# Performance work log

Measured on AMD Instinct MI355X. Metric: run time of the kernel, lower is better.

## Reference

```python
import jax, jax.numpy as jnp
import numpy as np

N, P, DEG, K, H, FIN, EPS = 65536, 64, 16, 3, 64, 16, 1e-5
E = N * DEG
G = N // P


def _bn(x, g, b):
    # BatchNorm1d, training mode: batch stats over the node dim
    mu = jnp.mean(x, axis=0)
    var = jnp.mean((x - mu) ** 2, axis=0)
    return g * (x - mu) * jax.lax.rsqrt(var + EPS) + b


def setup_inputs() -> dict:
    key = jax.random.key(0)
    ks = jax.random.split(key, 16)
    feat = jax.random.normal(ks[0], (N, FIN), jnp.float32)
    # 1024 graphs of 64 nodes, fixed in-degree DEG, edges stay within each graph
    dst = jnp.repeat(jnp.arange(N, dtype=jnp.int32), DEG)
    src = (dst // P) * P + jax.random.randint(ks[1], (E,), 0, P, jnp.int32)
    graph_ids = jnp.arange(N, dtype=jnp.int32) // P
    s = 0.1
    d = dict(feat=feat, src=src, dst=dst, graph_ids=graph_ids)
    d['cheb1_w'] = jax.random.normal(ks[2], (H, K * FIN), jnp.float32) * s
    d['cheb1_b'] = jnp.zeros((H,), jnp.float32)
    d['bn1_g'] = jnp.ones((H,), jnp.float32)
    d['bn1_b'] = jnp.zeros((H,), jnp.float32)
    d['e1_tw'] = jax.random.normal(ks[3], (H, H), jnp.float32) * s
    d['e1_tb'] = jnp.zeros((H,), jnp.float32)
    d['e1_pw'] = jax.random.normal(ks[4], (H, H), jnp.float32) * s
    d['e1_pb'] = jnp.zeros((H,), jnp.float32)
    d['bne1_g'] = jnp.ones((H,), jnp.float32)
    d['bne1_b'] = jnp.zeros((H,), jnp.float32)
    d['cheb2_w'] = jax.random.normal(ks[5], (H, K * H), jnp.float32) * s
    d['cheb2_b'] = jnp.zeros((H,), jnp.float32)
    d['bn2_g'] = jnp.ones((H,), jnp.float32)
    d['bn2_b'] = jnp.zeros((H,), jnp.float32)
    d['e2_tw'] = jax.random.normal(ks[6], (H, H), jnp.float32) * s
    d['e2_tb'] = jnp.zeros((H,), jnp.float32)
    d['e2_pw'] = jax.random.normal(ks[7], (H, H), jnp.float32) * s
    d['e2_pb'] = jnp.zeros((H,), jnp.float32)
    d['bne2_g'] = jnp.ones((H,), jnp.float32)
    d['bne2_b'] = jnp.zeros((H,), jnp.float32)
    d['cheb3_w'] = jax.random.normal(ks[8], (H, K * H), jnp.float32) * s
    d['cheb3_b'] = jnp.zeros((H,), jnp.float32)
    d['bn3_g'] = jnp.ones((H,), jnp.float32)
    d['bn3_b'] = jnp.zeros((H,), jnp.float32)
    return d


def _forward(feat, src, dst, graph_ids,
             cheb1_w, cheb1_b, bn1_g, bn1_b,
             e1_tw, e1_tb, e1_pw, e1_pb, bne1_g, bne1_b,
             cheb2_w, cheb2_b, bn2_g, bn2_b,
             e2_tw, e2_tb, e2_pw, e2_pb, bne2_g, bne2_b,
             cheb3_w, cheb3_b, bn3_g, bn3_b):
    # symmetric norm from in-degrees (DGL ChebConv), clamp(min=1)
    deg = jax.ops.segment_sum(jnp.ones((E,), jnp.float32), dst, num_segments=N)
    dinv = jnp.maximum(deg, 1.0) ** -0.5  # [N]
    dinv = dinv[:, None]

    def lap(f):  # A_hat @ f = D^-1/2 A D^-1/2 f  (messages src -> dst)
        return jax.ops.segment_sum((f * dinv)[src], dst, num_segments=N) * dinv

    def cheb(x, w, b):
        # lambda_max = 2 (DGL default) => re_norm = 1, L_hat = -A_hat
        X0 = x
        X1 = -lap(X0)
        Xs = [X0, X1]
        for _ in range(K - 2):
            Xi = -2.0 * lap(X1) - X0  # T_k = 2 L_hat T_{k-1} - T_{k-2}
            Xs.append(Xi)
            X0, X1 = X1, Xi
        return jnp.concatenate(Xs, axis=1) @ w.T + b

    def econv(x, tw, tb, pw, pb):
        # DGL EdgeConv: max_j [ theta(x_dst - x_src) + phi(x_dst) ]
        m = (x[dst] - x[src]) @ tw.T + tb + (x @ pw.T + pb)[dst]  # [E,H]
        agg = jax.ops.segment_max(m, dst, num_segments=N)
        return jnp.where(jnp.isfinite(agg), agg, 0.0)

    h = jax.nn.relu(_bn(cheb(feat, cheb1_w, cheb1_b), bn1_g, bn1_b))
    h = jax.nn.relu(_bn(econv(h, e1_tw, e1_tb, e1_pw, e1_pb), bne1_g, bne1_b))
    h = jax.nn.relu(_bn(cheb(h, cheb2_w, cheb2_b), bn2_g, bn2_b))
    h = jax.nn.relu(_bn(econv(h, e2_tw, e2_tb, e2_pw, e2_pb), bne2_g, bne2_b))
    h = jax.nn.relu(_bn(cheb(h, cheb3_w, cheb3_b), bn3_g, bn3_b))
    # dgl.mean_nodes: per-graph mean readout
    sums = jax.ops.segment_sum(h, graph_ids, num_segments=G)
    cnt = jax.ops.segment_sum(jnp.ones((N,), jnp.float32), graph_ids, num_segments=G)
    return sums / cnt[:, None]


def reference(feat, src, dst, graph_ids,
              cheb1_w, cheb1_b, bn1_g, bn1_b,
              e1_tw, e1_tb, e1_pw, e1_pb, bne1_g, bne1_b,
              cheb2_w, cheb2_b, bn2_g, bn2_b,
              e2_tw, e2_tb, e2_pw, e2_pb, bne2_g, bne2_b,
              cheb3_w, cheb3_b, bn3_g, bn3_b):
    return _forward(feat, src, dst, graph_ids,
                    cheb1_w, cheb1_b, bn1_g, bn1_b,
                    e1_tw, e1_tb, e1_pw, e1_pb, bne1_g, bne1_b,
                    cheb2_w, cheb2_b, bn2_g, bn2_b,
                    e2_tw, e2_tb, e2_pw, e2_pb, bne2_g, bne2_b,
                    cheb3_w, cheb3_b, bn3_g, bn3_b)
```

## Files before the change

### kernel.cpp

```cpp
#include <hip/hip_runtime.h>

#define NN 65536
#define PP 64
#define HH 64
#define FINN 16
#define NG 1024
#define EPSF 1e-5f
#define C1 0.0625f
#define NREP 32

typedef short bf16x8 __attribute__((ext_vector_type(8)));
typedef short s16x4 __attribute__((ext_vector_type(4)));
typedef float f32x4 __attribute__((ext_vector_type(4)));
typedef unsigned short u16;

#define MFMA(a, b, c) __builtin_amdgcn_mfma_f32_16x16x32_bf16(a, b, c, 0, 0, 0)

__device__ __forceinline__ u16 f2bf(float x) {
  union { float f; unsigned u; } v; v.f = x; return (u16)(v.u >> 16);
}
__device__ __forceinline__ float bf2f(u16 h) {
  union { float f; unsigned u; } v; v.u = ((unsigned)h) << 16; return v.f;
}
__device__ __forceinline__ void split2(float x, u16& h, u16& l) {
  h = f2bf(x); l = f2bf(x - bf2f(h));
}
__device__ __forceinline__ int XIDX(int r, int c) {
  return r * 64 + ((((c >> 3) ^ (r & 7)) << 3) | (c & 7));
}

__device__ __forceinline__ void rep_reduce(const float* __restrict__ stats_in,
                                           int t, float* sstats) {
  if (t < 128) {
    float s = 0.f;
    const float* p = stats_in + t;
#pragma unroll
    for (int r = 0; r < NREP; r++) s += p[r * 128];
    sstats[t] = s;
  }
}

__device__ __forceinline__ void build_adj(const int* __restrict__ src, int g,
                                          int r, u16* Adj) {
  bf16x8 z = {0, 0, 0, 0, 0, 0, 0, 0};
#pragma unroll
  for (int q = 0; q < 8; q++) *(bf16x8*)&Adj[r * 64 + q * 8] = z;
  const int4* s4 = (const int4*)(src + (size_t)g * 1024 + (size_t)r * 16);
  int4 a0 = s4[0], a1 = s4[1], a2 = s4[2], a3 = s4[3];
  int b0 = g * 64;
  int ss[16] = {a0.x - b0, a0.y - b0, a0.z - b0, a0.w - b0,
                a1.x - b0, a1.y - b0, a1.z - b0, a1.w - b0,
                a2.x - b0, a2.y - b0, a2.z - b0, a2.w - b0,
                a3.x - b0, a3.y - b0, a3.z - b0, a3.w - b0};
#pragma unroll
  for (int e = 0; e < 16; e++) {
    int idx = XIDX(r, ss[e]);
    Adj[idx] = f2bf(bf2f(Adj[idx]) + 1.0f);
  }
}

__device__ __forceinline__ void stage_load(const float* __restrict__ y_in,
                                           int g, int t, float4* v) {
  int n = t >> 2, c0 = (t & 3) * 16;
  const float* yr = y_in + ((size_t)(g * 64 + n)) * 64 + c0;
#pragma unroll
  for (int q = 0; q < 4; q++) v[q] = ((const float4*)yr)[q];
}

__device__ __forceinline__ void stage_bn2(
    const float4* v, const float* sstats, const float* __restrict__ gam,
    const float* __restrict__ bet, int t, u16* NMh, u16* NMl, u16* CMh,
    u16* CMl) {
  const float inv = 1.0f / (float)NN;
  int n = t >> 2, c0 = (t & 3) * 16;
  u16 hh[16], ll[16];
#pragma unroll
  for (int q = 0; q < 4; q++) {
#pragma unroll
    for (int k = 0; k < 4; k++) {
      int c = c0 + q * 4 + k;
      float s1 = sstats[c], s2 = sstats[64 + c];
      float mu = s1 * inv;
      float var = fmaf(s2, inv, -mu * mu);
      float sc = gam[c] * rsqrtf(var + EPSF);
      float sh = fmaf(-mu, sc, bet[c]);
      float x = (k == 0) ? v[q].x : (k == 1) ? v[q].y : (k == 2) ? v[q].z
                                                                 : v[q].w;
      float h = fmaxf(fmaf(sc, x, sh), 0.f);
      split2(h, hh[q * 4 + k], ll[q * 4 + k]);
    }
  }
  bf16x8 vh0, vh1, vl0, vl1;
#pragma unroll
  for (int k = 0; k < 8; k++) {
    vh0[k] = (short)hh[k]; vl0[k] = (short)ll[k];
    vh1[k] = (short)hh[8 + k]; vl1[k] = (short)ll[8 + k];
  }
  *(bf16x8*)&NMh[XIDX(n, c0)] = vh0;
  *(bf16x8*)&NMh[XIDX(n, c0 + 8)] = vh1;
  *(bf16x8*)&NMl[XIDX(n, c0)] = vl0;
  *(bf16x8*)&NMl[XIDX(n, c0 + 8)] = vl1;
  if (CMh) {
#pragma unroll
    for (int k = 0; k < 16; k++) {
      CMh[XIDX(c0 + k, n)] = hh[k];
      CMl[XIDX(c0 + k, n)] = ll[k];
    }
  }
}

__device__ __forceinline__ void epilogue(f32x4 a0, f32x4 a1, f32x4 a2, f32x4 a3,
                                         const float* __restrict__ bias, int g,
                                         int w, int ml, int kq,
                                         float* __restrict__ y_out,
                                         float* __restrict__ stats_out) {
  float4 bb = *(const float4*)(bias + w * 16 + kq * 4);
  float s1[4] = {0, 0, 0, 0}, s2[4] = {0, 0, 0, 0};
#pragma unroll
  for (int nt = 0; nt < 4; nt++) {
    f32x4 A = (nt == 0) ? a0 : (nt == 1) ? a1 : (nt == 2) ? a2 : a3;
    float4 yv;
    yv.x = A[0] + bb.x; yv.y = A[1] + bb.y;
    yv.z = A[2] + bb.z; yv.w = A[3] + bb.w;
    int n = nt * 16 + ml;
    *(float4*)(y_out + ((size_t)(g * 64 + n)) * 64 + w * 16 + kq * 4) = yv;
    s1[0] += yv.x; s2[0] += yv.x * yv.x;
    s1[1] += yv.y; s2[1] += yv.y * yv.y;
    s1[2] += yv.z; s2[2] += yv.z * yv.z;
    s1[3] += yv.w; s2[3] += yv.w * yv.w;
  }
#pragma unroll
  for (int i = 0; i < 4; i++) {
#pragma unroll
    for (int off = 1; off < 16; off <<= 1) {
      s1[i] += __shfl_xor(s1[i], off, 64);
      s2[i] += __shfl_xor(s2[i], off, 64);
    }
  }
  if (ml == 0) {
    float* pr = stats_out + (size_t)(g & (NREP - 1)) * 128 + w * 16 + kq * 4;
    atomicAdd(pr + 0, s1[0]);
    atomicAdd(pr + 1, s1[1]);
    atomicAdd(pr + 2, s1[2]);
    atomicAdd(pr + 3, s1[3]);
    atomicAdd(pr + 64, s2[0]);
    atomicAdd(pr + 65, s2[1]);
    atomicAdd(pr + 66, s2[2]);
    atomicAdd(pr + 67, s2[3]);
  }
}

__global__ __launch_bounds__(256, 2) void k_cheb64(
    const float* __restrict__ y_in, const float* __restrict__ stats_in,
    const float* __restrict__ gam, const float* __restrict__ bet,
    const int* __restrict__ src, const u16* __restrict__ wh,
    const u16* __restrict__ wl, const float* __restrict__ bias,
    float* __restrict__ y_out, float* __restrict__ stats_out) {
  __shared__ u16 NMh[4096], NMl[4096], C0h[4096], C0l[4096], C1h[4096],
      C1l[4096], Adj[4096];
  __shared__ float sstats[128];
  const int t = threadIdx.x, g = blockIdx.x;
  const int L = t & 63;
  const int w = __builtin_amdgcn_readfirstlane(t >> 6);
  const int ml = L & 15, kq = L >> 4;

  float4 yv4[4];
  stage_load(y_in, g, t, yv4);
  rep_reduce(stats_in, t, sstats);
  if (w == 3) build_adj(src, g, L, Adj);
  __syncthreads();
  stage_bn2(yv4, sstats, gam, bet, t, NMh, NMl, C0h, C0l);
  __syncthreads();

  f32x4 acc0 = {0, 0, 0, 0}, acc1 = {0, 0, 0, 0}, acc2 = {0, 0, 0, 0},
        acc3 = {0, 0, 0, 0};
  const u16* whp = wh + (size_t)(w * 16 + ml) * 192 + kq * 8;
  const u16* wlp = wl + (size_t)(w * 16 + ml) * 192 + kq * 8;

  auto yacc = [&](int kbase) {
#pragma unroll
    for (int kt = 0; kt < 2; kt++) {
      bf16x8 ah = *(const bf16x8*)(whp + kbase + kt * 32);
      bf16x8 al = *(const bf16x8*)(wlp + kbase + kt * 32);
      int kk = kt * 32 + kq * 8;
#pragma unroll
      for (int nt = 0; nt < 4; nt++) {
        int node = nt * 16 + ml;
        bf16x8 bh = *(const bf16x8*)&NMh[XIDX(node, kk)];
        bf16x8 bl = *(const bf16x8*)&NMl[XIDX(node, kk)];
        f32x4& A = (nt == 0) ? acc0 : (nt == 1) ? acc1 : (nt == 2) ? acc2 : acc3;
        A = MFMA(ah, bh, A);
        A = MFMA(al, bh, A);
        A = MFMA(ah, bl, A);
      }
    }
  };

  auto lap = [&](const u16* Bh, const u16* Bl, float scale, u16* oCh, u16* oCl) {
    f32x4 l0 = {0, 0, 0, 0}, l1 = {0, 0, 0, 0}, l2 = {0, 0, 0, 0},
          l3 = {0, 0, 0, 0};
#pragma unroll
    for (int kt = 0; kt < 2; kt++) {
      int kk = kt * 32 + kq * 8;
      bf16x8 aa = *(const bf16x8*)&Adj[XIDX(w * 16 + ml, kk)];
#pragma unroll
      for (int nt = 0; nt < 4; nt++) {
        bf16x8 bh = *(const bf16x8*)&Bh[XIDX(nt * 16 + ml, kk)];
        bf16x8 bl = *(const bf16x8*)&Bl[XIDX(nt * 16 + ml, kk)];
        f32x4& A = (nt == 0) ? l0 : (nt == 1) ? l1 : (nt == 2) ? l2 : l3;
        A = MFMA(aa, bh, A);
        A = MFMA(aa, bl, A);
      }
    }
    int r0 = w * 16 + kq * 4;
#pragma unroll
    for (int nt = 0; nt < 4; nt++) {
      f32x4 A = (nt == 0) ? l0 : (nt == 1) ? l1 : (nt == 2) ? l2 : l3;
      int c = nt * 16 + ml;
      u16 hh[4], ll[4];
#pragma unroll
      for (int i = 0; i < 4; i++) {
        split2(A[i] * scale, hh[i], ll[i]);
        NMh[XIDX(r0 + i, c)] = hh[i];
        NMl[XIDX(r0 + i, c)] = ll[i];
      }
      if (oCh) {
        s16x4 vh, vl;
#pragma unroll
        for (int i = 0; i < 4; i++) { vh[i] = (short)hh[i]; vl[i] = (short)ll[i]; }
        *(s16x4*)&oCh[XIDX(c, r0)] = vh;
        *(s16x4*)&oCl[XIDX(c, r0)] = vl;
      }
    }
  };

  yacc(0);
  __syncthreads();
  lap(C0h, C0l, -C1, C1h, C1l);
  __syncthreads();
  yacc(64);
  __syncthreads();
  lap(C1h, C1l, -2.0f * C1, nullptr, nullptr);
  __syncthreads();
  yacc(128);
  epilogue(acc0, acc1, acc2, acc3, bias, g, w, ml, kq, y_out, stats_out);
}

__global__ __launch_bounds__(256, 4) void k_econv(
    const float* __restrict__ y_in, const float* __restrict__ stats_in,
    const float* __restrict__ gam, const float* __restrict__ bet,
    const int* __restrict__ src, const u16* __restrict__ twh,
    const u16* __restrict__ twl, const u16* __restrict__ pwh,
    const u16* __restrict__ pwl, const float* __restrict__ tb,
    const float* __restrict__ pb, float* __restrict__ y_out,
    float* __restrict__ stats_out) {
  __shared__ u16 NMh[4096], NMl[4096];
  __shared__ float Tf[64 * 68];
  __shared__ unsigned sW[256];
  __shared__ float sstats[128];
  const int t = threadIdx.x, g = blockIdx.x;
  const int L = t & 63;
  const int w = __builtin_amdgcn_readfirstlane(t >> 6);
  const int ml = L & 15, kq = L >> 4;

  float4 yv4[4];
  stage_load(y_in, g, t, yv4);
  {
    const int4* s4 = (const int4*)(src + (size_t)g * 1024);
    int4 v = s4[t];
    int b0 = g * 64;
    sW[t] = (unsigned)(v.x - b0) | ((unsigned)(v.y - b0) << 8) |
            ((unsigned)(v.z - b0) << 16) | ((unsigned)(v.w - b0) << 24);
  }
  rep_reduce(stats_in, t, sstats);
  __syncthreads();
  stage_bn2(yv4, sstats, gam, bet, t, NMh, NMl, nullptr, nullptr);
  __syncthreads();

  f32x4 t0 = {0,0,0,0}, t1 = {0,0,0,0}, t2 = {0,0,0,0}, t3 = {0,0,0,0};
  f32x4 p0 = {0,0,0,0}, p1 = {0,0,0,0}, p2 = {0,0,0,0}, p3 = {0,0,0,0};
  const size_t wrow = (size_t)(w * 16 + ml) * 64 + kq * 8;
#pragma unroll
  for (int kt = 0; kt < 2; kt++) {
    bf16x8 ath = *(const bf16x8*)(twh + wrow + kt * 32);
    bf16x8 atl = *(const bf16x8*)(twl + wrow + kt * 32);
    bf16x8 aph = *(const bf16x8*)(pwh + wrow + kt * 32);
    bf16x8 apl = *(const bf16x8*)(pwl + wrow + kt * 32);
    int kk = kt * 32 + kq * 8;
#pragma unroll
    for (int nt = 0; nt < 4; nt++) {
      int node = nt * 16 + ml;
      bf16x8 bh = *(const bf16x8*)&NMh[XIDX(node, kk)];
      bf16x8 bl = *(const bf16x8*)&NMl[XIDX(node, kk)];
      f32x4& T = (nt == 0) ? t0 : (nt == 1) ? t1 : (nt == 2) ? t2 : t3;
      f32x4& P = (nt == 0) ? p0 : (nt == 1) ? p1 : (nt == 2) ? p2 : p3;
      T = MFMA(ath, bh, T); T = MFMA(atl, bh, T); T = MFMA(ath, bl, T);
      P = MFMA(aph, bh, P); P = MFMA(apl, bh, P); P = MFMA(aph, bl, P);
    }
  }
#pragma unroll
  for (int nt = 0; nt < 4; nt++) {
    f32x4 T = (nt == 0) ? t0 : (nt == 1) ? t1 : (nt == 2) ? t2 : t3;
    int n = nt * 16 + ml;
    float4 v; v.x = T[0]; v.y = T[1]; v.z = T[2]; v.w = T[3];
    *(float4*)&Tf[n * 68 + w * 16 + kq * 4] = v;
  }
  float4 tbv = *(const float4*)(tb + w * 16 + kq * 4);
  float4 pbv = *(const float4*)(pb + w * 16 + kq * 4);
  float s1[4] = {0, 0, 0, 0}, s2[4] = {0, 0, 0, 0};
#pragma unroll
  for (int nt = 0; nt < 4; nt++) {
    int n = nt * 16 + ml;
    unsigned w0 = sW[n * 4], w1 = sW[n * 4 + 1], w2 = sW[n * 4 + 2],
             w3 = sW[n * 4 + 3];
    float4 mn = {3.4e38f, 3.4e38f, 3.4e38f, 3.4e38f};
#pragma unroll
    for (int e = 0; e < 16; e++) {
      unsigned wd = (e < 4) ? w0 : (e < 8) ? w1 : (e < 12) ? w2 : w3;
      int s = (wd >> ((e & 3) * 8)) & 255;
      float4 tv = *(const float4*)&Tf[s * 68 + w * 16 + kq * 4];
      mn.x = fminf(mn.x, tv.x); mn.y = fminf(mn.y, tv.y);
      mn.z = fminf(mn.z, tv.z); mn.w = fminf(mn.w, tv.w);
    }
    f32x4 T = (nt == 0) ? t0 : (nt == 1) ? t1 : (nt == 2) ? t2 : t3;
    f32x4 P = (nt == 0) ? p0 : (nt == 1) ? p1 : (nt == 2) ? p2 : p3;
    float4 yv;
    yv.x = T[0] + P[0] + tbv.x + pbv.x - mn.x;
    yv.y = T[1] + P[1] + tbv.y + pbv.y - mn.y;
    yv.z = T[2] + P[2] + tbv.z + pbv.z - mn.z;
    yv.w = T[3] + P[3] + tbv.w + pbv.w - mn.w;
    *(float4*)(y_out + ((size_t)(g * 64 + n)) * 64 + w * 16 + kq * 4) = yv;
    s1[0] += yv.x; s2[0] += yv.x * yv.x;
    s1[1] += yv.y; s2[1] += yv.y * yv.y;
    s1[2] += yv.z; s2[2] += yv.z * yv.z;
    s1[3] += yv.w; s2[3] += yv.w * yv.w;
  }
#pragma unroll
  for (int i = 0; i < 4; i++) {
#pragma unroll
    for (int off = 1; off < 16; off <<= 1) {
      s1[i] += __shfl_xor(s1[i], off, 64);
      s2[i] += __shfl_xor(s2[i], off, 64);
    }
  }
  if (ml == 0) {
    float* pr = stats_out + (size_t)(g & (NREP - 1)) * 128 + w * 16 + kq * 4;
    atomicAdd(pr + 0, s1[0]);
    atomicAdd(pr + 1, s1[1]);
    atomicAdd(pr + 2, s1[2]);
    atomicAdd(pr + 3, s1[3]);
    atomicAdd(pr + 64, s2[0]);
    atomicAdd(pr + 65, s2[1]);
    atomicAdd(pr + 66, s2[2]);
    atomicAdd(pr + 67, s2[3]);
  }
}

__global__ __launch_bounds__(256, 3) void k_cheb1(
    const float* __restrict__ feat, const int* __restrict__ src,
    const u16* __restrict__ wh, const u16* __restrict__ wl,
    const float* __restrict__ bias, float* __restrict__ y_out,
    float* __restrict__ stats_out) {
  __shared__ u16 NMh[4096], NMl[4096], Ch[4096], Cl[4096], Adj[4096];
  const int t = threadIdx.x, g = blockIdx.x;
  const int L = t & 63;
  const int w = __builtin_amdgcn_readfirstlane(t >> 6);
  const int ml = L & 15, kq = L >> 4;
  {
    int n = t >> 2, c0 = (t & 3) * 4;
    float4 v = *(const float4*)(feat + (size_t)(g * 64 + n) * 16 + c0);
    u16 hh[4], ll[4];
    split2(v.x, hh[0], ll[0]); split2(v.y, hh[1], ll[1]);
    split2(v.z, hh[2], ll[2]); split2(v.w, hh[3], ll[3]);
    s16x4 vh, vl;
#pragma unroll
    for (int i = 0; i < 4; i++) { vh[i] = (short)hh[i]; vl[i] = (short)ll[i]; }
    *(s16x4*)&NMh[XIDX(n, c0)] = vh;
    *(s16x4*)&NMl[XIDX(n, c0)] = vl;
#pragma unroll
    for (int i = 0; i < 4; i++) {
      Ch[XIDX(c0 + i, n)] = hh[i];
      Cl[XIDX(c0 + i, n)] = ll[i];
    }
  }
  if (w == 0) {
    bf16x8 z = {0, 0, 0, 0, 0, 0, 0, 0};
    *(bf16x8*)&NMh[XIDX(L, 48)] = z;
    *(bf16x8*)&NMh[XIDX(L, 56)] = z;
  } else if (w == 1) {
    bf16x8 z = {0, 0, 0, 0, 0, 0, 0, 0};
    *(bf16x8*)&NMl[XIDX(L, 48)] = z;
    *(bf16x8*)&NMl[XIDX(L, 56)] = z;
  } else if (w == 3) {
    build_adj(src, g, L, Adj);
  }
  __syncthreads();

  {
    f32x4 l0 = {0, 0, 0, 0};
#pragma unroll
    for (int kt = 0; kt < 2; kt++) {
      int kk = kt * 32 + kq * 8;
      bf16x8 aa = *(const bf16x8*)&Adj[XIDX(w * 16 + ml, kk)];
      bf16x8 bh = *(const bf16x8*)&Ch[XIDX(ml, kk)];
      bf16x8 bl = *(const bf16x8*)&Cl[XIDX(ml, kk)];
      l0 = MFMA(aa, bh, l0);
      l0 = MFMA(aa, bl, l0);
    }
    int r0 = w * 16 + kq * 4;
    u16 hh[4], ll[4];
#pragma unroll
    for (int i = 0; i < 4; i++) {
      split2(l0[i] * (-C1), hh[i], ll[i]);
      NMh[XIDX(r0 + i, 16 + ml)] = hh[i];
      NMl[XIDX(r0 + i, 16 + ml)] = ll[i];
    }
    s16x4 vh, vl;
#pragma unroll
    for (int i = 0; i < 4; i++) { vh[i] = (short)hh[i]; vl[i] = (short)ll[i]; }
    *(s16x4*)&Ch[XIDX(16 + ml, r0)] = vh;
    *(s16x4*)&Cl[XIDX(16 + ml, r0)] = vl;
  }
  __syncthreads();
  {
    f32x4 l0 = {0, 0, 0, 0};
#pragma unroll
    for (int kt = 0; kt < 2; kt++) {
      int kk = kt * 32 + kq * 8;
      bf16x8 aa = *(const bf16x8*)&Adj[XIDX(w * 16 + ml, kk)];
      bf16x8 bh = *(const bf16x8*)&Ch[XIDX(16 + ml, kk)];
      bf16x8 bl = *(const bf16x8*)&Cl[XIDX(16 + ml, kk)];
      l0 = MFMA(aa, bh, l0);
      l0 = MFMA(aa, bl, l0);
    }
    int r0 = w * 16 + kq * 4;
    u16 hh[4], ll[4];
#pragma unroll
    for (int i = 0; i < 4; i++) {
      split2(l0[i] * (-2.0f * C1), hh[i], ll[i]);
      NMh[XIDX(r0 + i, 32 + ml)] = hh[i];
      NMl[XIDX(r0 + i, 32 + ml)] = ll[i];
    }
  }
  __syncthreads();
  f32x4 acc0 = {0,0,0,0}, acc1 = {0,0,0,0}, acc2 = {0,0,0,0}, acc3 = {0,0,0,0};
  const u16* whp = wh + (size_t)(w * 16 + ml) * 64 + kq * 8;
  const u16* wlp = wl + (size_t)(w * 16 + ml) * 64 + kq * 8;
#pragma unroll
  for (int kt = 0; kt < 2; kt++) {
    bf16x8 ah = *(const bf16x8*)(whp + kt * 32);
// ... 91 lines not shown
    split2(e1p[i], h, l); P1h[i] = h; P1l[i] = l;
    split2(e2t[i], h, l); T2h[i] = h; T2l[i] = l;
    split2(e2p[i], h, l); P2h[i] = h; P2l[i] = l;
  }
}

extern "C" void kernel_launch(void* const* d_in, const int* in_sizes, int n_in,
                              void* d_out, int out_size, void* d_ws,
                              size_t ws_size, hipStream_t stream) {
  const float* feat = (const float*)d_in[0];
  const int* src = (const int*)d_in[1];
  const float* cheb1_w = (const float*)d_in[4];
  const float* cheb1_b = (const float*)d_in[5];
  const float* bn1_g = (const float*)d_in[6];
  const float* bn1_b = (const float*)d_in[7];
  const float* e1_tw = (const float*)d_in[8];
  const float* e1_tb = (const float*)d_in[9];
  const float* e1_pw = (const float*)d_in[10];
  const float* e1_pb = (const float*)d_in[11];
  const float* bne1_g = (const float*)d_in[12];
  const float* bne1_b = (const float*)d_in[13];
  const float* cheb2_w = (const float*)d_in[14];
  const float* cheb2_b = (const float*)d_in[15];
  const float* bn2_g = (const float*)d_in[16];
  const float* bn2_b = (const float*)d_in[17];
  const float* e2_tw = (const float*)d_in[18];
  const float* e2_tb = (const float*)d_in[19];
  const float* e2_pw = (const float*)d_in[20];
  const float* e2_pb = (const float*)d_in[21];
  const float* bne2_g = (const float*)d_in[22];
  const float* bne2_b = (const float*)d_in[23];
  const float* cheb3_w = (const float*)d_in[24];
  const float* cheb3_b = (const float*)d_in[25];
  const float* bn3_g = (const float*)d_in[26];
  const float* bn3_b = (const float*)d_in[27];

  float* bufA = (float*)d_ws;
  float* bufB = bufA + (size_t)NN * HH;
  float* stats = bufB + (size_t)NN * HH;
  u16* wq = (u16*)(stats + 5 * NREP * 128);
  u16* W1h = wq;           u16* W1l = W1h + 4096;
  u16* W2h = W1l + 4096;   u16* W2l = W2h + 12288;
  u16* W3h = W2l + 12288;  u16* W3l = W3h + 12288;
  u16* T1h = W3l + 12288;  u16* T1l = T1h + 4096;
  u16* P1h = T1l + 4096;   u16* P1l = P1h + 4096;
  u16* T2h = P1l + 4096;   u16* T2l = T2h + 4096;
  u16* P2h = T2l + 4096;   u16* P2l = P2h + 4096;

  k_prep<<<16, 256, 0, stream>>>(cheb1_w, cheb2_w, cheb3_w, e1_tw, e1_pw,
                                 e2_tw, e2_pw, W1h, W1l, W2h, W2l, W3h, W3l,
                                 T1h, T1l, P1h, P1l, T2h, T2l, P2h, P2l,
                                 stats);

  k_cheb1<<<NG, 256, 0, stream>>>(feat, src, W1h, W1l, cheb1_b, bufA,
                                  stats + 0 * NREP * 128);
  k_econv<<<NG, 256, 0, stream>>>(bufA, stats + 0 * NREP * 128, bn1_g, bn1_b,
                                  src, T1h, T1l, P1h, P1l, e1_tb, e1_pb, bufB,
                                  stats + 1 * NREP * 128);
  k_cheb64<<<NG, 256, 0, stream>>>(bufB, stats + 1 * NREP * 128, bne1_g,
                                   bne1_b, src, W2h, W2l, cheb2_b, bufA,
                                   stats + 2 * NREP * 128);
  k_econv<<<NG, 256, 0, stream>>>(bufA, stats + 2 * NREP * 128, bn2_g, bn2_b,
                                  src, T2h, T2l, P2h, P2l, e2_tb, e2_pb, bufB,
                                  stats + 3 * NREP * 128);
  k_cheb64<<<NG, 256, 0, stream>>>(bufB, stats + 3 * NREP * 128, bne2_g,
                                   bne2_b, src, W3h, W3l, cheb3_b, bufA,
                                   stats + 4 * NREP * 128);
  k_pool<<<NG, 256, 0, stream>>>(bufA, stats + 4 * NREP * 128, bn3_g, bn3_b,
                                 (float*)d_out);
}
```

Measured before the change: 216.7 us.

## Fuse all GNN layers into one cooperative persistent kernel with grid syncs

Replaces six per-layer kernel launches with a single cooperative kernel of 512 blocks, each owning two graphs. Activations stay in registers across layers, and a grid-wide barrier separates layers so the global BatchNorm statistics are complete before they are used. This removes the activation round-trips through global memory and the launch gaps between kernels. In exchange it adds grid synchronisation cost, requires two resident blocks per CU under the launch bounds, and falls back to the old path if cooperative launch is unavailable.

```diff
diff --git a/kernel.cpp b/kernel.cpp
--- a/kernel.cpp
+++ b/kernel.cpp
@@ -1,10 +1,14 @@
 #include <hip/hip_runtime.h>
+#include <hip/hip_cooperative_groups.h>
+
+namespace cg = cooperative_groups;
 
 #define NN 65536
 #define PP 64
 #define HH 64
 #define FINN 16
 #define NG 1024
+#define NBLK 512
 #define EPSF 1e-5f
 #define C1 0.0625f
 #define NREP 32
@@ -27,17 +31,6 @@
 }
 __device__ __forceinline__ int XIDX(int r, int c) {
   return r * 64 + ((((c >> 3) ^ (r & 7)) << 3) | (c & 7));
-}
-
-__device__ __forceinline__ void rep_reduce(const float* __restrict__ stats_in,
-                                           int t, float* sstats) {
-  if (t < 128) {
-    float s = 0.f;
-    const float* p = stats_in + t;
-#pragma unroll
-    for (int r = 0; r < NREP; r++) s += p[r * 128];
-    sstats[t] = s;
-  }
 }
 
 __device__ __forceinline__ void build_adj(const int* __restrict__ src, int g,
@@ -56,6 +49,454 @@
   for (int e = 0; e < 16; e++) {
     int idx = XIDX(r, ss[e]);
     Adj[idx] = f2bf(bf2f(Adj[idx]) + 1.0f);
+  }
+}
+
+struct KP {
+  const float* feat; const int* src;
+  const u16 *W1h, *W1l, *W2h, *W2l, *W3h, *W3l;
+  const u16 *T1h, *T1l, *P1h, *P1l, *T2h, *T2l, *P2h, *P2l;
+  const float *c1b, *bn1g, *bn1b;
+  const float *e1tb, *e1pb, *bne1g, *bne1b;
+  const float *c2b, *bn2g, *bn2b;
+  const float *e2tb, *e2pb, *bne2g, *bne2b;
+  const float *c3b, *bn3g, *bn3b;
+  float* stats;
+  float* out;
+};
+
+__global__ __launch_bounds__(256, 2) void k_fused(KP p) {
+  __shared__ __align__(16) u16 SH[28672];
+  __shared__ float sstats[128];
+  u16* NMh = SH;
+  u16* NMl = SH + 4096;
+  u16* X0h = SH + 8192;
+  u16* X0l = SH + 12288;
+  u16* X1h = SH + 16384;
+  u16* X1l = SH + 20480;
+  u16* Adj = SH + 24576;
+  float* Tf = (float*)(SH + 8192);
+  unsigned* sW = (unsigned*)(SH + 20480);
+
+  const int t = threadIdx.x;
+  const int L = t & 63;
+  const int w = __builtin_amdgcn_readfirstlane(t >> 6);
+  const int ml = L & 15, kq = L >> 4;
+  const int c0 = w * 16 + kq * 4;
+
+  f32x4 ya[4], yb[4];
+  const int ga = blockIdx.x * 2, gb = ga + 1;
+
+  cg::grid_group grid = cg::this_grid();
+  auto gsync = [&]() { __threadfence(); grid.sync(); };
+
+  auto rep_red = [&](const float* sb) {
+    if (t < 128) {
+      float s = 0.f;
+#pragma unroll
+      for (int r = 0; r < NREP; r++)
+        s += __hip_atomic_load(sb + (size_t)r * 128 + t, __ATOMIC_RELAXED,
+                               __HIP_MEMORY_SCOPE_AGENT);
+      sstats[t] = s;
+    }
+  };
+
+  auto stats_acc = [&](f32x4 (&y)[4], int g, float* so) {
+    float s1[4] = {0, 0, 0, 0}, s2[4] = {0, 0, 0, 0};
+#pragma unroll
+    for (int nt = 0; nt < 4; nt++)
+#pragma unroll
+      for (int i = 0; i < 4; i++) {
+        s1[i] += y[nt][i];
+        s2[i] += y[nt][i] * y[nt][i];
+      }
+#pragma unroll
+    for (int i = 0; i < 4; i++)
+#pragma unroll
+      for (int off = 1; off < 16; off <<= 1) {
+        s1[i] += __shfl_xor(s1[i], off, 64);
+        s2[i] += __shfl_xor(s2[i], off, 64);
+      }
+    if (ml == 0) {
+      float* pr = so + (size_t)(g & (NREP - 1)) * 128 + c0;
+#pragma unroll
+      for (int i = 0; i < 4; i++) {
+        atomicAdd(pr + i, s1[i]);
+        atomicAdd(pr + 64 + i, s2[i]);
+      }
+    }
+  };
+
+  auto bn_frag = [&](f32x4 (&y)[4], const float* gam, const float* bet,
+                     u16* CMh, u16* CMl) {
+    const float inv = 1.0f / (float)NN;
+    float sc[4], sh[4];
+#pragma unroll
+    for (int i = 0; i < 4; i++) {
+      int c = c0 + i;
+      float s1 = sstats[c], s2 = sstats[64 + c];
+      float mu = s1 * inv;
+      float var = fmaf(s2, inv, -mu * mu);
+      sc[i] = gam[c] * rsqrtf(var + EPSF);
+      sh[i] = fmaf(-mu, sc[i], bet[c]);
+    }
+#pragma unroll
+    for (int nt = 0; nt < 4; nt++) {
+      int node = nt * 16 + ml;
+      u16 hh[4], ll[4];
+      s16x4 vh, vl;
+#pragma unroll
+      for (int i = 0; i < 4; i++) {
+        float h = fmaxf(fmaf(sc[i], y[nt][i], sh[i]), 0.f);
+        split2(h, hh[i], ll[i]);
+        vh[i] = (short)hh[i]; vl[i] = (short)ll[i];
+      }
+      *(s16x4*)&NMh[XIDX(node, c0)] = vh;
+      *(s16x4*)&NMl[XIDX(node, c0)] = vl;
+      if (CMh) {
+#pragma unroll
+        for (int i = 0; i < 4; i++) {
+          CMh[XIDX(c0 + i, node)] = hh[i];
+          CMl[XIDX(c0 + i, node)] = ll[i];
+        }
+      }
+    }
+  };
+
+  auto cheb64_graph = [&](int g, f32x4 (&y)[4], const u16* wh, const u16* wl,
+                          const float* bias, const float* gam,
+                          const float* bet, float* so) {
+    bn_frag(y, gam, bet, X0h, X0l);
+    if (w == 3) build_adj(p.src, g, L, Adj);
+    __syncthreads();
+
+    f32x4 acc[4] = {};
+    auto yacc = [&](int kbase) {
+      const u16* whp = wh + (size_t)(w * 16 + ml) * 192 + kq * 8 + kbase;
+      const u16* wlp = wl + (size_t)(w * 16 + ml) * 192 + kq * 8 + kbase;
+#pragma unroll
+      for (int kt = 0; kt < 2; kt++) {
+        bf16x8 ah = *(const bf16x8*)(whp + kt * 32);
+        bf16x8 al = *(const bf16x8*)(wlp + kt * 32);
+        int kk = kt * 32 + kq * 8;
+#pragma unroll
+        for (int nt = 0; nt < 4; nt++) {
+          bf16x8 bh = *(const bf16x8*)&NMh[XIDX(nt * 16 + ml, kk)];
+          bf16x8 bl = *(const bf16x8*)&NMl[XIDX(nt * 16 + ml, kk)];
+          acc[nt] = MFMA(ah, bh, acc[nt]);
+          acc[nt] = MFMA(al, bh, acc[nt]);
+          acc[nt] = MFMA(ah, bl, acc[nt]);
+        }
+      }
+    };
+    auto lap = [&](const u16* Bh, const u16* Bl, float scale, u16* oCh,
+                   u16* oCl) {
+      f32x4 l[4] = {};
+#pragma unroll
+      for (int kt = 0; kt < 2; kt++) {
+        int kk = kt * 32 + kq * 8;
+        bf16x8 aa = *(const bf16x8*)&Adj[XIDX(w * 16 + ml, kk)];
+#pragma unroll
+        for (int nt = 0; nt < 4; nt++) {
+          bf16x8 bh = *(const bf16x8*)&Bh[XIDX(nt * 16 + ml, kk)];
+          bf16x8 bl = *(const bf16x8*)&Bl[XIDX(nt * 16 + ml, kk)];
+          l[nt] = MFMA(aa, bh, l[nt]);
+          l[nt] = MFMA(aa, bl, l[nt]);
+        }
+      }
+      int r0 = w * 16 + kq * 4;
+#pragma unroll
+      for (int nt = 0; nt < 4; nt++) {
+        int c = nt * 16 + ml;
+        u16 hh[4], ll[4];
+#pragma unroll
+        for (int i = 0; i < 4; i++) {
+          split2(l[nt][i] * scale, hh[i], ll[i]);
+          NMh[XIDX(r0 + i, c)] = hh[i];
+          NMl[XIDX(r0 + i, c)] = ll[i];
+        }
+        if (oCh) {
+          s16x4 vh, vl;
+#pragma unroll
+          for (int i = 0; i < 4; i++) {
+            vh[i] = (short)hh[i]; vl[i] = (short)ll[i];
+          }
+          *(s16x4*)&oCh[XIDX(c, r0)] = vh;
+          *(s16x4*)&oCl[XIDX(c, r0)] = vl;
+        }
+      }
+    };
+
+    yacc(0);
+    __syncthreads();
+    lap(X0h, X0l, -C1, X1h, X1l);
+    __syncthreads();
+    yacc(64);
+    __syncthreads();
+    lap(X1h, X1l, -2.0f * C1, nullptr, nullptr);
+    __syncthreads();
+    yacc(128);
+    float4 bb = *(const float4*)(bias + c0);
+#pragma unroll
+    for (int nt = 0; nt < 4; nt++) {
+      y[nt][0] = acc[nt][0] + bb.x;
+      y[nt][1] = acc[nt][1] + bb.y;
+      y[nt][2] = acc[nt][2] + bb.z;
+      y[nt][3] = acc[nt][3] + bb.w;
+    }
+    stats_acc(y, g, so);
+  };
+
+  auto econv_graph = [&](int g, f32x4 (&y)[4], const u16* twh, const u16* twl,
+                         const u16* pwh, const u16* pwl, const float* tb,
+                         const float* pb, const float* gam, const float* bet,
+                         float* so) {
+    bn_frag(y, gam, bet, nullptr, nullptr);
+    {
+      int4 v = ((const int4*)(p.src + (size_t)g * 1024))[t];
+      int b0 = g * 64;
+      sW[t] = (unsigned)(v.x - b0) | ((unsigned)(v.y - b0) << 8) |
+              ((unsigned)(v.z - b0) << 16) | ((unsigned)(v.w - b0) << 24);
+    }
+    __syncthreads();
+
+    f32x4 tA[4] = {}, pA[4] = {};
+    const size_t wrow = (size_t)(w * 16 + ml) * 64 + kq * 8;
+#pragma unroll
+    for (int kt = 0; kt < 2; kt++) {
+      bf16x8 ath = *(const bf16x8*)(twh + wrow + kt * 32);
+      bf16x8 atl = *(const bf16x8*)(twl + wrow + kt * 32);
+      bf16x8 aph = *(const bf16x8*)(pwh + wrow + kt * 32);
+      bf16x8 apl = *(const bf16x8*)(pwl + wrow + kt * 32);
+      int kk = kt * 32 + kq * 8;
+#pragma unroll
+      for (int nt = 0; nt < 4; nt++) {
+        bf16x8 bh = *(const bf16x8*)&NMh[XIDX(nt * 16 + ml, kk)];
+        bf16x8 bl = *(const bf16x8*)&NMl[XIDX(nt * 16 + ml, kk)];
+        tA[nt] = MFMA(ath, bh, tA[nt]);
+        tA[nt] = MFMA(atl, bh, tA[nt]);
+        tA[nt] = MFMA(ath, bl, tA[nt]);
+        pA[nt] = MFMA(aph, bh, pA[nt]);
+        pA[nt] = MFMA(apl, bh, pA[nt]);
+        pA[nt] = MFMA(aph, bl, pA[nt]);
+      }
+    }
+#pragma unroll
+    for (int nt = 0; nt < 4; nt++) {
+      int n = nt * 16 + ml;
+      float4 v;
+      v.x = tA[nt][0]; v.y = tA[nt][1]; v.z = tA[nt][2]; v.w = tA[nt][3];
+      *(float4*)&Tf[n * 68 + c0] = v;
+    }
+    float4 tbv = *(const float4*)(tb + c0);
+    float4 pbv = *(const float4*)(pb + c0);
+#pragma unroll
+    for (int nt = 0; nt < 4; nt++) {
+      int n = nt * 16 + ml;
+      unsigned w0 = sW[n * 4], w1 = sW[n * 4 + 1], w2 = sW[n * 4 + 2],
+               w3 = sW[n * 4 + 3];
+      float4 mn = {3.4e38f, 3.4e38f, 3.4e38f, 3.4e38f};
+#pragma unroll
+      for (int e = 0; e < 16; e++) {
+        unsigned wd = (e < 4) ? w0 : (e < 8) ? w1 : (e < 12) ? w2 : w3;
+        int s = (wd >> ((e & 3) * 8)) & 255;
+        float4 tv = *(const float4*)&Tf[s * 68 + c0];
+        mn.x = fminf(mn.x, tv.x); mn.y = fminf(mn.y, tv.y);
+        mn.z = fminf(mn.z, tv.z); mn.w = fminf(mn.w, tv.w);
+      }
+      y[nt][0] = tA[nt][0] + pA[nt][0] + tbv.x + pbv.x - mn.x;
+      y[nt][1] = tA[nt][1] + pA[nt][1] + tbv.y + pbv.y - mn.y;
+      y[nt][2] = tA[nt][2] + pA[nt][2] + tbv.z + pbv.z - mn.z;
+      y[nt][3] = tA[nt][3] + pA[nt][3] + tbv.w + pbv.w - mn.w;
+    }
+    stats_acc(y, g, so);
+  };
+
+  auto cheb1_graph = [&](int g, f32x4 (&y)[4]) {
+    {
+      int n = t >> 2, cc = (t & 3) * 4;
+      float4 v = *(const float4*)(p.feat + (size_t)(g * 64 + n) * 16 + cc);
+      u16 hh[4], ll[4];
+      split2(v.x, hh[0], ll[0]); split2(v.y, hh[1], ll[1]);
+      split2(v.z, hh[2], ll[2]); split2(v.w, hh[3], ll[3]);
+      s16x4 vh, vl;
+#pragma unroll
+      for (int i = 0; i < 4; i++) { vh[i] = (short)hh[i]; vl[i] = (short)ll[i]; }
+      *(s16x4*)&NMh[XIDX(n, cc)] = vh;
+      *(s16x4*)&NMl[XIDX(n, cc)] = vl;
+#pragma unroll
+      for (int i = 0; i < 4; i++) {
+        X0h[XIDX(cc + i, n)] = hh[i];
+        X0l[XIDX(cc + i, n)] = ll[i];
+      }
+    }
+    if (w == 0) {
+      bf16x8 z = {0, 0, 0, 0, 0, 0, 0, 0};
+      *(bf16x8*)&NMh[XIDX(L, 48)] = z;
+      *(bf16x8*)&NMh[XIDX(L, 56)] = z;
+    } else if (w == 1) {
+      bf16x8 z = {0, 0, 0, 0, 0, 0, 0, 0};
+      *(bf16x8*)&NMl[XIDX(L, 48)] = z;
+      *(bf16x8*)&NMl[XIDX(L, 56)] = z;
+    } else if (w == 3) {
+      build_adj(p.src, g, L, Adj);
+    }
+    __syncthreads();
+    {
+      f32x4 l0 = {};
+#pragma unroll
+      for (int kt = 0; kt < 2; kt++) {
+        int kk = kt * 32 + kq * 8;
+        bf16x8 aa = *(const bf16x8*)&Adj[XIDX(w * 16 + ml, kk)];
+        bf16x8 bh = *(const bf16x8*)&X0h[XIDX(ml, kk)];
+        bf16x8 bl = *(const bf16x8*)&X0l[XIDX(ml, kk)];
+        l0 = MFMA(aa, bh, l0);
+        l0 = MFMA(aa, bl, l0);
+      }
+      int r0 = w * 16 + kq * 4;
+      u16 hh[4], ll[4];
+#pragma unroll
+      for (int i = 0; i < 4; i++) {
+        split2(l0[i] * (-C1), hh[i], ll[i]);
+        NMh[XIDX(r0 + i, 16 + ml)] = hh[i];
+        NMl[XIDX(r0 + i, 16 + ml)] = ll[i];
+      }
+      s16x4 vh, vl;
+#pragma unroll
+      for (int i = 0; i < 4; i++) { vh[i] = (short)hh[i]; vl[i] = (short)ll[i]; }
+      *(s16x4*)&X0h[XIDX(16 + ml, r0)] = vh;
+      *(s16x4*)&X0l[XIDX(16 + ml, r0)] = vl;
+    }
+    __syncthreads();
+    {
+      f32x4 l0 = {};
+#pragma unroll
+      for (int kt = 0; kt < 2; kt++) {
+        int kk = kt * 32 + kq * 8;
+        bf16x8 aa = *(const bf16x8*)&Adj[XIDX(w * 16 + ml, kk)];
+        bf16x8 bh = *(const bf16x8*)&X0h[XIDX(16 + ml, kk)];
+        bf16x8 bl = *(const bf16x8*)&X0l[XIDX(16 + ml, kk)];
+        l0 = MFMA(aa, bh, l0);
+        l0 = MFMA(aa, bl, l0);
+      }
+      int r0 = w * 16 + kq * 4;
+      u16 hh[4], ll[4];
+#pragma unroll
+      for (int i = 0; i < 4; i++) {
+        split2(l0[i] * (-2.0f * C1), hh[i], ll[i]);
+        NMh[XIDX(r0 + i, 32 + ml)] = hh[i];
+        NMl[XIDX(r0 + i, 32 + ml)] = ll[i];
+      }
+    }
+    __syncthreads();
+    f32x4 acc[4] = {};
+    const u16* whp = p.W1h + (size_t)(w * 16 + ml) * 64 + kq * 8;
+    const u16* wlp = p.W1l + (size_t)(w * 16 + ml) * 64 + kq * 8;
+#pragma unroll
+    for (int kt = 0; kt < 2; kt++) {
+      bf16x8 ah = *(const bf16x8*)(whp + kt * 32);
+      bf16x8 al = *(const bf16x8*)(wlp + kt * 32);
+      int kk = kt * 32 + kq * 8;
+#pragma unroll
+      for (int nt = 0; nt < 4; nt++) {
+        bf16x8 bh = *(const bf16x8*)&NMh[XIDX(nt * 16 + ml, kk)];
+        bf16x8 bl = *(const bf16x8*)&NMl[XIDX(nt * 16 + ml, kk)];
+        acc[nt] = MFMA(ah, bh, acc[nt]);
+        acc[nt] = MFMA(al, bh, acc[nt]);
+        acc[nt] = MFMA(ah, bl, acc[nt]);
+      }
+    }
+    float4 bb = *(const float4*)(p.c1b + c0);
+#pragma unroll
+    for (int nt = 0; nt < 4; nt++) {
+      y[nt][0] = acc[nt][0] + bb.x;
+      y[nt][1] = acc[nt][1] + bb.y;
+      y[nt][2] = acc[nt][2] + bb.z;
+      y[nt][3] = acc[nt][3] + bb.w;
+    }
+    stats_acc(y, g, p.stats);
+  };
+
+  auto pool_graph = [&](int g, f32x4 (&y)[4], const float* gam,
+                        const float* bet) {
+    const float inv = 1.0f / (float)NN;
+    float sc[4], sh[4];
+#pragma unroll
+    for (int i = 0; i < 4; i++) {
+      int c = c0 + i;
+      float s1 = sstats[c], s2 = sstats[64 + c];
+      float mu = s1 * inv;
+      float var = fmaf(s2, inv, -mu * mu);
+      sc[i] = gam[c] * rsqrtf(var + EPSF);
+      sh[i] = fmaf(-mu, sc[i], bet[c]);
+    }
+    float s[4] = {0, 0, 0, 0};
+#pragma unroll
+    for (int nt = 0; nt < 4; nt++)
+#pragma unroll
+      for (int i = 0; i < 4; i++)
+        s[i] += fmaxf(fmaf(sc[i], y[nt][i], sh[i]), 0.f);
+#pragma unroll
+    for (int i = 0; i < 4; i++)
+#pragma unroll
+      for (int off = 1; off < 16; off <<= 1) s[i] += __shfl_xor(s[i], off, 64);
+    if (ml == 0) {
+      float4 o = make_float4(s[0] * (1.f / 64.f), s[1] * (1.f / 64.f),
+                             s[2] * (1.f / 64.f), s[3] * (1.f / 64.f));
+      *(float4*)(p.out + (size_t)g * 64 + c0) = o;
+    }
+  };
+
+  cheb1_graph(ga, ya);
+  __syncthreads();
+  cheb1_graph(gb, yb);
+  gsync();
+  rep_red(p.stats + 0);
+  __syncthreads();
+  econv_graph(ga, ya, p.T1h, p.T1l, p.P1h, p.P1l, p.e1tb, p.e1pb, p.bn1g,
+              p.bn1b, p.stats + (size_t)1 * NREP * 128);
+  __syncthreads();
+  econv_graph(gb, yb, p.T1h, p.T1l, p.P1h, p.P1l, p.e1tb, p.e1pb, p.bn1g,
+              p.bn1b, p.stats + (size_t)1 * NREP * 128);
+  gsync();
+  rep_red(p.stats + (size_t)1 * NREP * 128);
+  __syncthreads();
+  cheb64_graph(ga, ya, p.W2h, p.W2l, p.c2b, p.bne1g, p.bne1b,
+               p.stats + (size_t)2 * NREP * 128);
+  __syncthreads();
+  cheb64_graph(gb, yb, p.W2h, p.W2l, p.c2b, p.bne1g, p.bne1b,
+               p.stats + (size_t)2 * NREP * 128);
+  gsync();
+  rep_red(p.stats + (size_t)2 * NREP * 128);
+  __syncthreads();
+  econv_graph(ga, ya, p.T2h, p.T2l, p.P2h, p.P2l, p.e2tb, p.e2pb, p.bn2g,
+              p.bn2b, p.stats + (size_t)3 * NREP * 128);
+  __syncthreads();
+  econv_graph(gb, yb, p.T2h, p.T2l, p.P2h, p.P2l, p.e2tb, p.e2pb, p.bn2g,
+              p.bn2b, p.stats + (size_t)3 * NREP * 128);
+  gsync();
+  rep_red(p.stats + (size_t)3 * NREP * 128);
+  __syncthreads();
+  cheb64_graph(ga, ya, p.W3h, p.W3l, p.c3b, p.bne2g, p.bne2b,
+               p.stats + (size_t)4 * NREP * 128);
+  __syncthreads();
+  cheb64_graph(gb, yb, p.W3h, p.W3l, p.c3b, p.bne2g, p.bne2b,
+               p.stats + (size_t)4 * NREP * 128);
+  gsync();
+  rep_red(p.stats + (size_t)4 * NREP * 128);
+  __syncthreads();
+  pool_graph(ga, ya, p.bn3g, p.bn3b);
+  pool_graph(gb, yb, p.bn3g, p.bn3b);
+}
+
+__device__ __forceinline__ void rep_reduce(const float* __restrict__ stats_in,
+                                           int t, float* sstats) {
+  if (t < 128) {
+    float s = 0.f;
+    const float* p = stats_in + t;
+#pragma unroll
+    for (int r = 0; r < NREP; r++) s += p[r * 128];
+    sstats[t] = s;
   }
 }
 
@@ -395,7 +836,6 @@
     build_adj(src, g, L, Adj);
   }
   __syncthreads();
-
   {
     f32x4 l0 = {0, 0, 0, 0};
 #pragma unroll
@@ -593,20 +1033,51 @@
                                  T1h, T1l, P1h, P1l, T2h, T2l, P2h, P2l,
                                  stats);
 
-  k_cheb1<<<NG, 256, 0, stream>>>(feat, src, W1h, W1l, cheb1_b, bufA,
-                                  stats + 0 * NREP * 128);
-  k_econv<<<NG, 256, 0, stream>>>(bufA, stats + 0 * NREP * 128, bn1_g, bn1_b,
-                                  src, T1h, T1l, P1h, P1l, e1_tb, e1_pb, bufB,
-                                  stats + 1 * NREP * 128);
-  k_cheb64<<<NG, 256, 0, stream>>>(bufB, stats + 1 * NREP * 128, bne1_g,
-                                   bne1_b, src, W2h, W2l, cheb2_b, bufA,
-                                   stats + 2 * NREP * 128);
-  k_econv<<<NG, 256, 0, stream>>>(bufA, stats + 2 * NREP * 128, bn2_g, bn2_b,
-                                  src, T2h, T2l, P2h, P2l, e2_tb, e2_pb, bufB,
-                                  stats + 3 * NREP * 128);
-  k_cheb64<<<NG, 256, 0, stream>>>(bufB, stats + 3 * NREP * 128, bne2_g,
-                                   bne2_b, src, W3h, W3l, cheb3_b, bufA,
-                                   stats + 4 * NREP * 128);
-  k_pool<<<NG, 256, 0, stream>>>(bufA, stats + 4 * NREP * 128, bn3_g, bn3_b,
-                                 (float*)d_out);
-}
+  static int coop = -1;
+  if (coop < 0) {
+    int v = 0;
+    if (hipDeviceGetAttribute(&v, hipDeviceAttributeCooperativeLaunch, 0) !=
+        hipSuccess)
+      v = 0;
+    coop = v;
+  }
+
+  bool launched = false;
+  if (coop) {
+    KP p;
+    p.feat = feat; p.src = src;
+    p.W1h = W1h; p.W1l = W1l; p.W2h = W2h; p.W2l = W2l; p.W3h = W3h; p.W3l = W3l;
+    p.T1h = T1h; p.T1l = T1l; p.P1h = P1h; p.P1l = P1l;
+    p.T2h = T2h; p.T2l = T2l; p.P2h = P2h; p.P2l = P2l;
+    p.c1b = cheb1_b; p.bn1g = bn1_g; p.bn1b = bn1_b;
+    p.e1tb = e1_tb; p.e1pb = e1_pb; p.bne1g = bne1_g; p.bne1b = bne1_b;
+    p.c2b = cheb2_b; p.bn2g = bn2_g; p.bn2b = bn2_b;
+    p.e2tb = e2_tb; p.e2pb = e2_pb; p.bne2g = bne2_g; p.bne2b = bne2_b;
+    p.c3b = cheb3_b; p.bn3g = bn3_g; p.bn3b = bn3_b;
+    p.stats = stats; p.out = (float*)d_out;
+    void* args[] = {&p};
+    hipError_t e = hipLaunchCooperativeKernel(
+        reinterpret_cast<void*>(k_fused), dim3(NBLK), dim3(256), args, 0,
+        stream);
+    launched = (e == hipSuccess);
+  }
+
+  if (!launched) {
+    k_cheb1<<<NG, 256, 0, stream>>>(feat, src, W1h, W1l, cheb1_b, bufA,
+                                    stats + 0 * NREP * 128);
+    k_econv<<<NG, 256, 0, stream>>>(bufA, stats + 0 * NREP * 128, bn1_g, bn1_b,
+                                    src, T1h, T1l, P1h, P1l, e1_tb, e1_pb,
+                                    bufB, stats + 1 * NREP * 128);
+    k_cheb64<<<NG, 256, 0, stream>>>(bufB, stats + 1 * NREP * 128, bne1_g,
+                                     bne1_b, src, W2h, W2l, cheb2_b, bufA,
+                                     stats + 2 * NREP * 128);
+    k_econv<<<NG, 256, 0, stream>>>(bufA, stats + 2 * NREP * 128, bn2_g, bn2_b,
+                                    src, T2h, T2l, P2h, P2l, e2_tb, e2_pb,
+                                    bufB, stats + 3 * NREP * 128);
+    k_cheb64<<<NG, 256, 0, stream>>>(bufB, stats + 3 * NREP * 128, bne2_g,
+                                     bne2_b, src, W3h, W3l, cheb3_b, bufA,
+                                     stats + 4 * NREP * 128);
+    k_pool<<<NG, 256, 0, stream>>>(bufA, stats + 4 * NREP * 128, bn3_g, bn3_b,
+                                   (float*)d_out);
+  }
+}
```

After: 677.6 us. 213% more time.

## Shrink cheb64 shared memory by reusing buffers to raise occupancy

Applied to the files above, without the earlier changes.

The 64-wide Chebyshev kernel now packs its shared buffers into a single 40 KB array. The two C buffers are merged into one CM buffer that the first Laplacian step overwrites in place after an extra barrier, and the stats scratch is aliased onto the adjacency area. Loads are remapped so each thread loads and normalizes the columns matching its MFMA layout. Launch bounds rise to 4 blocks per CU for cheb64 and cheb1, trading a barrier and register pressure for higher occupancy.

```diff
diff --git a/kernel.cpp b/kernel.cpp
--- a/kernel.cpp
+++ b/kernel.cpp
@@ -29,17 +29,6 @@
   return r * 64 + ((((c >> 3) ^ (r & 7)) << 3) | (c & 7));
 }
 
-__device__ __forceinline__ void rep_reduce(const float* __restrict__ stats_in,
-                                           int t, float* sstats) {
-  if (t < 128) {
-    float s = 0.f;
-    const float* p = stats_in + t;
-#pragma unroll
-    for (int r = 0; r < NREP; r++) s += p[r * 128];
-    sstats[t] = s;
-  }
-}
-
 __device__ __forceinline__ void build_adj(const int* __restrict__ src, int g,
                                           int r, u16* Adj) {
   bf16x8 z = {0, 0, 0, 0, 0, 0, 0, 0};
@@ -59,6 +48,17 @@
   }
 }
 
+__device__ __forceinline__ void rep_reduce(const float* __restrict__ stats_in,
+                                           int t, float* sstats) {
+  if (t < 128) {
+    float s = 0.f;
+    const float* p = stats_in + t;
+#pragma unroll
+    for (int r = 0; r < NREP; r++) s += p[r * 128];
+    sstats[t] = s;
+  }
+}
+
 __device__ __forceinline__ void stage_load(const float* __restrict__ y_in,
                                            int g, int t, float4* v) {
   int n = t >> 2, c0 = (t & 3) * 16;
@@ -69,8 +69,7 @@
 
 __device__ __forceinline__ void stage_bn2(
     const float4* v, const float* sstats, const float* __restrict__ gam,
-    const float* __restrict__ bet, int t, u16* NMh, u16* NMl, u16* CMh,
-    u16* CMl) {
+    const float* __restrict__ bet, int t, u16* NMh, u16* NMl) {
   const float inv = 1.0f / (float)NN;
   int n = t >> 2, c0 = (t & 3) * 16;
   u16 hh[16], ll[16];
@@ -100,13 +99,6 @@
   *(bf16x8*)&NMh[XIDX(n, c0 + 8)] = vh1;
   *(bf16x8*)&NMl[XIDX(n, c0)] = vl0;
   *(bf16x8*)&NMl[XIDX(n, c0 + 8)] = vl1;
-  if (CMh) {
-#pragma unroll
-    for (int k = 0; k < 16; k++) {
-      CMh[XIDX(c0 + k, n)] = hh[k];
-      CMl[XIDX(c0 + k, n)] = ll[k];
-    }
-  }
 }
 
 __device__ __forceinline__ void epilogue(f32x4 a0, f32x4 a1, f32x4 a2, f32x4 a3,
@@ -150,30 +142,72 @@
   }
 }
 
-__global__ __launch_bounds__(256, 2) void k_cheb64(
+__global__ __launch_bounds__(256, 4) void k_cheb64(
     const float* __restrict__ y_in, const float* __restrict__ stats_in,
     const float* __restrict__ gam, const float* __restrict__ bet,
     const int* __restrict__ src, const u16* __restrict__ wh,
     const u16* __restrict__ wl, const float* __restrict__ bias,
     float* __restrict__ y_out, float* __restrict__ stats_out) {
-  __shared__ u16 NMh[4096], NMl[4096], C0h[4096], C0l[4096], C1h[4096],
-      C1l[4096], Adj[4096];
-  __shared__ float sstats[128];
+  __shared__ __align__(16) u16 SH[20480];
+  u16* NMh = SH;
+  u16* NMl = SH + 4096;
+  u16* CMh = SH + 8192;
+  u16* CMl = SH + 12288;
+  u16* Adj = SH + 16384;
+  float* sstats = (float*)(SH + 16384);
+
   const int t = threadIdx.x, g = blockIdx.x;
   const int L = t & 63;
   const int w = __builtin_amdgcn_readfirstlane(t >> 6);
   const int ml = L & 15, kq = L >> 4;
-
-  float4 yv4[4];
-  stage_load(y_in, g, t, yv4);
+  const int c0 = w * 16 + kq * 4;
+
+  float4 yv[4];
+#pragma unroll
+  for (int nt = 0; nt < 4; nt++)
+    yv[nt] =
+        *(const float4*)(y_in + ((size_t)(g * 64 + nt * 16 + ml)) * 64 + c0);
   rep_reduce(stats_in, t, sstats);
+  __syncthreads();
+  float sc[4], sh[4];
+  {
+    const float inv = 1.0f / (float)NN;
+#pragma unroll
+    for (int i = 0; i < 4; i++) {
+      int c = c0 + i;
+      float s1 = sstats[c], s2 = sstats[64 + c];
+      float mu = s1 * inv;
+      float var = fmaf(s2, inv, -mu * mu);
+      sc[i] = gam[c] * rsqrtf(var + EPSF);
+      sh[i] = fmaf(-mu, sc[i], bet[c]);
+    }
+  }
+  __syncthreads();
+
+#pragma unroll
+  for (int nt = 0; nt < 4; nt++) {
+    int node = nt * 16 + ml;
+    u16 hh[4], ll[4];
+    s16x4 vh, vl;
+    float xs[4] = {yv[nt].x, yv[nt].y, yv[nt].z, yv[nt].w};
+#pragma unroll
+    for (int i = 0; i < 4; i++) {
+      float h = fmaxf(fmaf(sc[i], xs[i], sh[i]), 0.f);
+      split2(h, hh[i], ll[i]);
+      vh[i] = (short)hh[i]; vl[i] = (short)ll[i];
+    }
+    *(s16x4*)&NMh[XIDX(node, c0)] = vh;
+    *(s16x4*)&NMl[XIDX(node, c0)] = vl;
+#pragma unroll
+    for (int i = 0; i < 4; i++) {
+      CMh[XIDX(c0 + i, node)] = hh[i];
+      CMl[XIDX(c0 + i, node)] = ll[i];
+    }
+  }
   if (w == 3) build_adj(src, g, L, Adj);
   __syncthreads();
-  stage_bn2(yv4, sstats, gam, bet, t, NMh, NMl, C0h, C0l);
-  __syncthreads();
-
-  f32x4 acc0 = {0, 0, 0, 0}, acc1 = {0, 0, 0, 0}, acc2 = {0, 0, 0, 0},
-        acc3 = {0, 0, 0, 0};
+
+  f32x4 acc[4] = {};
   const u16* whp = wh + (size_t)(w * 16 + ml) * 192 + kq * 8;
   const u16* wlp = wl + (size_t)(w * 16 + ml) * 192 + kq * 8;
 
@@ -185,65 +219,61 @@
       int kk = kt * 32 + kq * 8;
 #pragma unroll
       for (int nt = 0; nt < 4; nt++) {
-        int node = nt * 16 + ml;
-        bf16x8 bh = *(const bf16x8*)&NMh[XIDX(node, kk)];
-        bf16x8 bl = *(const bf16x8*)&NMl[XIDX(node, kk)];
-        f32x4& A = (nt == 0) ? acc0 : (nt == 1) ? acc1 : (nt == 2) ? acc2 : acc3;
-        A = MFMA(ah, bh, A);
-        A = MFMA(al, bh, A);
-        A = MFMA(ah, bl, A);
+        bf16x8 bh = *(const bf16x8*)&NMh[XIDX(nt * 16 + ml, kk)];
+        bf16x8 bl = *(const bf16x8*)&NMl[XIDX(nt * 16 + ml, kk)];
+        acc[nt] = MFMA(ah, bh, acc[nt]);
+        acc[nt] = MFMA(al, bh, acc[nt]);
+        acc[nt] = MFMA(ah, bl, acc[nt]);
       }
     }
   };
-
-  auto lap = [&](const u16* Bh, const u16* Bl, float scale, u16* oCh, u16* oCl) {
-    f32x4 l0 = {0, 0, 0, 0}, l1 = {0, 0, 0, 0}, l2 = {0, 0, 0, 0},
-          l3 = {0, 0, 0, 0};
+  auto lap = [&](float scale, bool writeCM) {
+    f32x4 l[4] = {};
 #pragma unroll
     for (int kt = 0; kt < 2; kt++) {
       int kk = kt * 32 + kq * 8;
       bf16x8 aa = *(const bf16x8*)&Adj[XIDX(w * 16 + ml, kk)];
 #pragma unroll
       for (int nt = 0; nt < 4; nt++) {
-        bf16x8 bh = *(const bf16x8*)&Bh[XIDX(nt * 16 + ml, kk)];
-        bf16x8 bl = *(const bf16x8*)&Bl[XIDX(nt * 16 + ml, kk)];
-        f32x4& A = (nt == 0) ? l0 : (nt == 1) ? l1 : (nt == 2) ? l2 : l3;
-        A = MFMA(aa, bh, A);
-        A = MFMA(aa, bl, A);
+        bf16x8 bh = *(const bf16x8*)&CMh[XIDX(nt * 16 + ml, kk)];
+        bf16x8 bl = *(const bf16x8*)&CMl[XIDX(nt * 16 + ml, kk)];
+        l[nt] = MFMA(aa, bh, l[nt]);
+        l[nt] = MFMA(aa, bl, l[nt]);
       }
     }
+    if (writeCM) __syncthreads();
     int r0 = w * 16 + kq * 4;
 #pragma unroll
     for (int nt = 0; nt < 4; nt++) {
-      f32x4 A = (nt == 0) ? l0 : (nt == 1) ? l1 : (nt == 2) ? l2 : l3;
       int c = nt * 16 + ml;
       u16 hh[4], ll[4];
 #pragma unroll
       for (int i = 0; i < 4; i++) {
-        split2(A[i] * scale, hh[i], ll[i]);
+        split2(l[nt][i] * scale, hh[i], ll[i]);
         NMh[XIDX(r0 + i, c)] = hh[i];
         NMl[XIDX(r0 + i, c)] = ll[i];
       }
-      if (oCh) {
+      if (writeCM) {
         s16x4 vh, vl;
 #pragma unroll
         for (int i = 0; i < 4; i++) { vh[i] = (short)hh[i]; vl[i] = (short)ll[i]; }
-        *(s16x4*)&oCh[XIDX(c, r0)] = vh;
-        *(s16x4*)&oCl[XIDX(c, r0)] = vl;
+        *(s16x4*)&CMh[XIDX(c, r0)] = vh;
+        *(s16x4*)&CMl[XIDX(c, r0)] = vl;
       }
     }
   };
 
   yacc(0);
   __syncthreads();
-  lap(C0h, C0l, -C1, C1h, C1l);
+  lap(-C1, true);
   __syncthreads();
   yacc(64);
   __syncthreads();
-  lap(C1h, C1l, -2.0f * C1, nullptr, nullptr);
+  lap(-2.0f * C1, false);
   __syncthreads();
   yacc(128);
-  epilogue(acc0, acc1, acc2, acc3, bias, g, w, ml, kq, y_out, stats_out);
+  epilogue(acc[0], acc[1], acc[2], acc[3], bias, g, w, ml, kq, y_out,
+           stats_out);
 }
 
 __global__ __launch_bounds__(256, 4) void k_econv(
@@ -274,7 +304,7 @@
   }
   rep_reduce(stats_in, t, sstats);
   __syncthreads();
-  stage_bn2(yv4, sstats, gam, bet, t, NMh, NMl, nullptr, nullptr);
+  stage_bn2(yv4, sstats, gam, bet, t, NMh, NMl);
   __syncthreads();
 
   f32x4 t0 = {0,0,0,0}, t1 = {0,0,0,0}, t2 = {0,0,0,0}, t3 = {0,0,0,0};
@@ -356,7 +386,7 @@
   }
 }
 
-__global__ __launch_bounds__(256, 3) void k_cheb1(
+__global__ __launch_bounds__(256, 4) void k_cheb1(
     const float* __restrict__ feat, const int* __restrict__ src,
     const u16* __restrict__ wh, const u16* __restrict__ wl,
     const float* __restrict__ bias, float* __restrict__ y_out,
```

After: 210.1 us, median of 2. 3.0% less time.
